# Optimization experiments

Hardware: AMD Instinct MI355X
Metric: run time of the kernel (lower is better)

The kernel has to match this reference:

```python
import jax, jax.numpy as jnp
import numpy as np

RES = 28          # resolution (H == W)
DIM = 384         # channels
NH = 8            # num_heads
HD = DIM // NH    # head_dim = 48
N = RES * RES     # tokens = 784
B = 16            # batch


def _build_bias_idxs(res):
    # Faithful reproduction of the first-occurrence offset indexing in __init__.
    pts = [(i, j) for i in range(res) for j in range(res)]
    offs = {}
    idxs = []
    for p1 in pts:
        for p2 in pts:
            o = (abs(p1[0] - p2[0]), abs(p1[1] - p2[1]))
            if o not in offs:
                offs[o] = len(offs)
            idxs.append(offs[o])
    return np.asarray(idxs, dtype=np.int32).reshape(res * res, res * res), len(offs)


def setup_inputs() -> dict:
    key = jax.random.key(0)
    ks = jax.random.split(key, 6)
    idxs, noff = _build_bias_idxs(RES)  # noff == RES*RES == 784
    s = 0.02
    return {
        "ll": jax.random.normal(ks[0], (B, DIM, RES, RES), jnp.float32),
        "high_attn": jax.random.normal(ks[1], (B, DIM, RES, RES), jnp.float32),
        # 1x1 convs stored as [out_ch, in_ch] matrices
        "q_w": jax.random.normal(ks[2], (DIM, DIM), jnp.float32) * s,
        "q_b": jnp.zeros((DIM,), jnp.float32),
        "kv_w": jax.random.normal(ks[3], (2 * DIM, DIM), jnp.float32) * s,
        "kv_b": jnp.zeros((2 * DIM,), jnp.float32),
        "proj_w": jax.random.normal(ks[4], (DIM, DIM), jnp.float32) * s,
        "proj_b": jnp.zeros((DIM,), jnp.float32),
        "attn_biases": jax.random.normal(ks[5], (NH, noff), jnp.float32) * s,
        "bias_idxs": jnp.asarray(idxs),  # [N, N] int32
    }


def reference(ll, high_attn, q_w, q_b, kv_w, kv_b, proj_w, proj_b, attn_biases, bias_idxs):
    b, c, h, w = ll.shape
    n = h * w
    scale = HD ** -0.5
    # 1x1 convs == per-pixel channel matmuls
    q = jnp.einsum('bchw,oc->bohw', ll, q_w) + q_b[:, None, None]
    kv = jnp.einsum('bchw,oc->bohw', high_attn, kv_w) + kv_b[:, None, None]
    k, v = jnp.split(kv, 2, axis=1)
    q = q.reshape(b, NH, HD, n).transpose(0, 1, 3, 2)  # [B,H,N,hd]
    k = k.reshape(b, NH, HD, n)                        # [B,H,hd,N]
    v = v.reshape(b, NH, HD, n).transpose(0, 1, 3, 2)  # [B,H,N,hd]
    attn = jnp.einsum('bhnd,bhdm->bhnm', q, k) * scale  # [B,H,N,N]
    bias = attn_biases[:, bias_idxs]                    # gather -> [H,N,N]
    attn = jax.nn.softmax(attn + bias[None], axis=-1)
    out = jnp.einsum('bhnm,bhmd->bhnd', attn, v)        # [B,H,N,hd]
    out = out.transpose(0, 1, 3, 2).reshape(b, c, h, w)
    return jnp.einsum('bchw,oc->bohw', out, proj_w) + proj_b[:, None, None]
```

## Files before the change

kernel.cpp:

```cpp
#include <hip/hip_runtime.h>

#define RES    28
#define DIMC   384
#define NHEAD  8
#define HDIM   48
#define DPAD   64
#define NPIX   784
#define NB     16
#define SC2    0.20823294f
#define LOG2E  1.44269504f

typedef short bf16x8 __attribute__((ext_vector_type(8)));
typedef float f32x4  __attribute__((ext_vector_type(4)));

__device__ __forceinline__ short f2bf(float x) {
  union { float f; unsigned u; } v; v.f = x;
  return (short)((v.u + 0x7FFFu + ((v.u >> 16) & 1u)) >> 16);
}
__device__ __forceinline__ unsigned pk_rne(float a, float b) {
  union { float f; unsigned u; } x, y; x.f = a; y.f = b;
  return __builtin_amdgcn_perm(y.u + 0x7FFFu + ((y.u >> 16) & 1u),
                               x.u + 0x7FFFu + ((x.u >> 16) & 1u), 0x07060302u);
}
__device__ __forceinline__ unsigned pk_hu(float a, float b) {
  union { float f; unsigned u; } x, y; x.f = a; y.f = b;
  return __builtin_amdgcn_perm(y.u + 0x8000u, x.u + 0x8000u, 0x07060302u);
}
__device__ __forceinline__ float blo(unsigned u) { union { unsigned u; float f; } v; v.u = u << 16; return v.f; }
__device__ __forceinline__ float bhi(unsigned u) { union { unsigned u; float f; } v; v.u = u & 0xFFFF0000u; return v.f; }


__global__ __launch_bounds__(256) void prep_kernel(
    const float* __restrict__ ll, const float* __restrict__ ha,
    const float* __restrict__ qw, const float* __restrict__ kvw, const float* __restrict__ pw,
    const float* __restrict__ biases,
    short* __restrict__ Xll, short* __restrict__ Xha,
    short* __restrict__ Wf2, short* __restrict__ Wfp,
    short* __restrict__ Bt3, short* __restrict__ Qb,
    short* __restrict__ Kf, short* __restrict__ Vf)
{
  __shared__ __align__(16) short sT[64][72];
  __shared__ float sB[NPIX];
  const int bid = blockIdx.x, t = threadIdx.x;

  if (bid < 2496) {
    const int px = bid % 13, cb = (bid / 13) % 6, zz = bid / 78;
    const int which = zz >> 4, b = zz & 15;
    const float* X = (which ? ha : ll) + (size_t)b * DIMC * NPIX;
    short* T = (which ? Xha : Xll);
    const int c0 = cb * 64, p0 = px * 64;
    const int rrr = t >> 4, pc = (t & 15) * 4;
#pragma unroll
    for (int i = 0; i < 4; ++i) {
      const int c = rrr + 16 * i;
      if (p0 + pc < NPIX) {
        float4 v = *(const float4*)(X + (size_t)(c0 + c) * NPIX + p0 + pc);
        sT[pc + 0][c] = f2bf(v.x); sT[pc + 1][c] = f2bf(v.y);
        sT[pc + 2][c] = f2bf(v.z); sT[pc + 3][c] = f2bf(v.w);
      }
    }
    __syncthreads();
    const int rr = t & 15, qq = (t >> 4) & 3, w = t >> 6;
    const int pxt0 = p0 >> 4, ks0 = c0 >> 5;
#pragma unroll
    for (int i = 0; i < 2; ++i) {
      const int o = w * 2 + i;
      const int pxl = o >> 1, ksl = o & 1;
      if (pxt0 + pxl < 49) {
        short* dst = T + ((size_t)(b * 49 + pxt0 + pxl) * 12 + ks0 + ksl) * 512 + (t & 63) * 8;
        *(bf16x8*)dst = *(const bf16x8*)&sT[pxl * 16 + rr][ksl * 32 + qq * 8];
      }
    }
  } else if (bid < 2784) {
    int gid = (bid - 2496) * 256 + t;
    if (gid < 55296) {
      const int lane = gid & 63;
      const int mt = (gid >> 6) & 7;
      const int ks = (gid >> 9) % 12;
      const int ct = gid / 6144;
      const int chg = ct * 128 + mt * 16 + (lane & 15);
      const int k = ks * 32 + (lane >> 4) * 8;
      const float* src = (chg < DIMC ? qw + (size_t)chg * DIMC
                                     : kvw + (size_t)(chg - DIMC) * DIMC) + k;
      const float4 a = *(const float4*)src;
      const float4 b = *(const float4*)(src + 4);
      bf16x8 o;
      o[0] = f2bf(a.x); o[1] = f2bf(a.y); o[2] = f2bf(a.z); o[3] = f2bf(a.w);
      o[4] = f2bf(b.x); o[5] = f2bf(b.y); o[6] = f2bf(b.z); o[7] = f2bf(b.w);
      *(bf16x8*)(Wf2 + (size_t)gid * 8) = o;
    } else {
      const int g2 = gid - 55296;
      const int lane = g2 & 63;
      const int ks = (g2 >> 6) % 12;
      const int mtile = g2 / 768;
      const int row = mtile * 16 + (lane & 15);
      const int k = ks * 32 + (lane >> 4) * 8;
      const float* src = pw + (size_t)row * DIMC + k;
      const float4 a = *(const float4*)src;
      const float4 b = *(const float4*)(src + 4);
      bf16x8 o;
      o[0] = f2bf(a.x); o[1] = f2bf(a.y); o[2] = f2bf(a.z); o[3] = f2bf(a.w);
      o[4] = f2bf(b.x); o[5] = f2bf(b.y); o[6] = f2bf(b.z); o[7] = f2bf(b.w);
      *(bf16x8*)(Wfp + (size_t)g2 * 8) = o;
    }
  } else if (bid < 3176) {
    const int bb = bid - 2784;
    const int h = bb / 49, qt = bb % 49;
    for (int i = t; i < NPIX; i += 256) sB[i] = biases[h * NPIX + i] * LOG2E;
    __syncthreads();
    const int rr = t & 15, qq = (t >> 4) & 3, w = t >> 6;
    const int qrow = qt * 16 + rr;
    const int i2 = qrow / RES, j2 = qrow - i2 * RES;
    short* dst0 = Bt3 + ((size_t)(h * 49 + qt) * 25) * 512 + (t & 63) * 8;
    const short NEG = f2bf(-1e30f);
    for (int c = w; c < 25; c += 4) {
      short v8[8];
#pragma unroll
      for (int hf = 0; hf < 2; ++hf)
#pragma unroll
        for (int u = 0; u < 4; ++u) {
          const int k = c * 32 + hf * 16 + qq * 4 + u;
          if (k < NPIX) {
            const int i1 = k / RES, j1 = k - i1 * RES;
            int di = i1 - i2; di = di < 0 ? -di : di;
            int dj = j1 - j2; dj = dj < 0 ? -dj : dj;
            v8[hf * 4 + u] = f2bf(sB[di * RES + dj]);
          } else v8[hf * 4 + u] = NEG;
        }
      *(bf16x8*)(dst0 + (size_t)c * 512) = *(const bf16x8*)v8;
    }
  } else {
    const int pp = bid - 3176;
    if (pp < 392) {
      const size_t r = (size_t)pp * 256 + t;
      short* p = Qb + r * DPAD + HDIM;
      *(int4*)p = make_int4(0, 0, 0, 0);
      *(int4*)(p + 8) = make_int4(0, 0, 0, 0);
    } else if (pp < 1192) {
      const int id = (pp - 392) * 256 + t;
      const int l32 = id & 31;
      const int frag = 1 + 2 * ((id >> 5) & 1);
      const int chunk = (id >> 6) % 25;
      const int bh2 = id / 1600;
      short* dst = Kf + (((size_t)bh2 * 25 + chunk) * 4 + frag) * 512 + (32 + l32) * 8;
      *(int4*)dst = make_int4(0, 0, 0, 0);
    } else if (pp < 1256) {
      const int id = (pp - 1192) * 256 + t;
      const int lane2 = id & 63;
      const int frag = 2 + ((id >> 6) & 1);
      const int bh2 = id >> 7;
      short* dst = Kf + (((size_t)bh2 * 25 + 24) * 4 + frag) * 512 + lane2 * 8;
      *(int4*)dst = make_int4(0, 0, 0, 0);
    } else {
      const int id = (pp - 1256) * 256 + t;
      const int bh2 = id / 96;
      const int rem = id - bh2 * 96;
      const int frag = rem >> 5;
      const int l32 = rem & 31;
      short* dst = Vf + (((size_t)bh2 * 25 + 24) * 3 + frag) * 512 + (32 + l32) * 8;
      *(int4*)dst = make_int4(0, 0, 0, 0);
    }
  }
}

__global__ __launch_bounds__(256) void qkv_tiled(
    const short* __restrict__ Wf2, const float* __restrict__ qb, const float* __restrict__ kvb,
    const short* __restrict__ Xll, const short* __restrict__ Xha,
    short* __restrict__ Qb, short* __restrict__ Kf, short* __restrict__ Vf)
{
  __shared__ __align__(16) short sM[15360];
  const int t = threadIdx.x;
  const int w = t >> 6, lane = t & 63;
  const int rr = lane & 15, qq = lane >> 4;
  const int ct = blockIdx.x;
  const int pt = blockIdx.y;
  const int b = pt / 7, pt7 = pt % 7;
  const int px0 = pt7 * 112;

  const short* Xsel = (ct < 3 ? Xll : Xha);
  const short* Bp[7];
#pragma unroll
  for (int pg = 0; pg < 7; ++pg)
    Bp[pg] = Xsel + ((size_t)(b * 49 + pt7 * 7 + pg) * 12) * 512 + lane * 8;

  const short* Ap = Wf2 + (size_t)ct * 12 * 4096 + 2 * w * 512 + lane * 8;

  f32x4 acc[2][7];
#pragma unroll
  for (int mi = 0; mi < 2; ++mi)
#pragma unroll
    for (int pg = 0; pg < 7; ++pg) acc[mi][pg] = (f32x4){0.f, 0.f, 0.f, 0.f};

  bf16x8 a0c = *(const bf16x8*)(Ap);
  bf16x8 a1c = *(const bf16x8*)(Ap + 512);
  bf16x8 bcur[7];
#pragma unroll
  for (int pg = 0; pg < 7; ++pg) bcur[pg] = *(const bf16x8*)(Bp[pg]);

#pragma unroll 2
  for (int s = 0; s < 12; ++s) {
    const int sn = s + (s < 11 ? 1 : 0);
    const short* an = Ap + (size_t)sn * 4096;
    bf16x8 a0n = *(const bf16x8*)(an);
    bf16x8 a1n = *(const bf16x8*)(an + 512);
    bf16x8 bnxt[7];
#pragma unroll
    for (int pg = 0; pg < 7; ++pg) bnxt[pg] = *(const bf16x8*)(Bp[pg] + sn * 512);

#pragma unroll
    for (int pg = 0; pg < 7; ++pg) {
      acc[0][pg] = __builtin_amdgcn_mfma_f32_16x16x32_bf16(a0c, bcur[pg], acc[0][pg], 0, 0, 0);
      acc[1][pg] = __builtin_amdgcn_mfma_f32_16x16x32_bf16(a1c, bcur[pg], acc[1][pg], 0, 0, 0);
    }
    a0c = a0n; a1c = a1n;
#pragma unroll
    for (int pg = 0; pg < 7; ++pg) bcur[pg] = bnxt[pg];
  }

  if (ct < 3) {
#pragma unroll
    for (int mi = 0; mi < 2; ++mi) {
      const int ch = ct * 128 + (2 * w + mi) * 16 + qq * 4;
      const float4 bv = *(const float4*)(qb + ch);
      const int hh = ch / HDIM, d0 = ch % HDIM;
#pragma unroll
      for (int pg = 0; pg < 7; ++pg) {
        const int px = px0 + pg * 16 + rr;
        uint2 pk;
        pk.x = pk_rne(acc[mi][pg][0] + bv.x, acc[mi][pg][1] + bv.y);
        pk.y = pk_rne(acc[mi][pg][2] + bv.z, acc[mi][pg][3] + bv.w);
        *(uint2*)(Qb + (((size_t)b * NHEAD + hh) * NPIX + px) * DPAD + d0) = pk;
      }
    }
  } else if (ct < 6) {
#pragma unroll
    for (int mi = 0; mi < 2; ++mi) {
      const int ch = (ct - 3) * 128 + (2 * w + mi) * 16 + qq * 4;
      const float4 bv = *(const float4*)(kvb + ch);
      const int hh = ch / HDIM, dq = ch % HDIM;
      const int fd = dq >> 5;
      const int laneHi = (dq & 31) >> 3;
      const int elo = dq & 7;
#pragma unroll
      for (int pg = 0; pg < 7; ++pg) {
        const int px = px0 + pg * 16 + rr;
        const int chunk = px >> 5, kh = (px >> 4) & 1;
        uint2 pk;
        pk.x = pk_rne(acc[mi][pg][0] + bv.x, acc[mi][pg][1] + bv.y);
        pk.y = pk_rne(acc[mi][pg][2] + bv.z, acc[mi][pg][3] + bv.w);
        short* dst = Kf + ((((size_t)b * NHEAD + hh) * 25 + chunk) * 4 + kh * 2 + fd) * 512
                     + ((px & 15) + (laneHi << 4)) * 8 + elo;
        *(uint2*)dst = pk;
      }
    }
  } else {
#pragma unroll
    for (int mi = 0; mi < 2; ++mi) {
      const int chl = (2 * w + mi) * 16 + qq * 4;
      const int chv = (ct - 6) * 128 + chl;
      const float4 bv = *(const float4*)(kvb + DIMC + chv);
      const float bb[4] = {bv.x, bv.y, bv.z, bv.w};
#pragma unroll
      for (int pg = 0; pg < 7; ++pg) {
        const int px = pg * 16 + rr;
#pragma unroll
        for (int j = 0; j < 4; ++j)
          sM[(chl + j) * 120 + px] = f2bf(acc[mi][pg][j] + bb[j]);
      }
    }
    __syncthreads();
    for (int id = t; id < 1792; id += 256) {
      const int r = id / 14, o = id - r * 14;
      const int k = px0 + o * 8;
      const int chunk = k >> 5, qv = (k >> 3) & 3;
      const int chv = (ct - 6) * 128 + r;
      const int hh = chv / HDIM, d = chv % HDIM;
      short* dst = Vf + ((((size_t)b * NHEAD + hh) * 25 + chunk) * 3 + (d >> 4)) * 512
                   + ((d & 15) + (qv << 4)) * 8;
      *(bf16x8*)dst = *(const bf16x8*)&sM[r * 120 + o * 8];
    }
  }
}

struct Chain { float sp; f32x4 O0, O1, O2; };

__device__ __forceinline__ void chain_init(Chain& c) {
  c.sp = 0.f;
  c.O0 = (f32x4){0.f,0.f,0.f,0.f}; c.O1 = c.O0; c.O2 = c.O0;
}

__device__ __forceinline__ void chain_step(
    Chain& c, const f32x4 d0, const f32x4 d1, const uint2 bw0, const uint2 bw1,
    short* sPt, const int rr, const int qq)
{
  float s[8];
  s[0] = fmaf(d0[0], SC2, blo(bw0.x)); s[1] = fmaf(d0[1], SC2, bhi(bw0.x));
  s[2] = fmaf(d0[2], SC2, blo(bw0.y)); s[3] = fmaf(d0[3], SC2, bhi(bw0.y));
  s[4] = fmaf(d1[0], SC2, blo(bw1.x)); s[5] = fmaf(d1[1], SC2, bhi(bw1.x));
  s[6] = fmaf(d1[2], SC2, blo(bw1.y)); s[7] = fmaf(d1[3], SC2, bhi(bw1.y));
  float p[8];
#pragma unroll
  for (int j = 0; j < 8; ++j) p[j] = exp2f(fminf(s[j], 30.f));
  const float ss = ((p[0] + p[1]) + (p[2] + p[3])) + ((p[4] + p[5]) + (p[6] + p[7]));
  c.sp += ss;
  uint2 w0; w0.x = pk_hu(p[0], p[1]); w0.y = pk_hu(p[2], p[3]);
  uint2 w1; w1.x = pk_hu(p[4], p[5]); w1.y = pk_hu(p[6], p[7]);
  *(uint2*)(sPt + rr * 40 + qq * 4) = w0;
  *(uint2*)(sPt + rr * 40 + 16 + qq * 4) = w1;
}

__global__ __launch_bounds__(256) void attn_kernel(
    const short* __restrict__ Q, const short* __restrict__ Kf,
    const short* __restrict__ Vf, const short* __restrict__ Bt3,
    short* __restrict__ AOf)
{
  __shared__ __align__(16) char sMem[20480];
  short* sPbase = (short*)sMem;
  const int t = threadIdx.x;
  const int w = t >> 6, lane = t & 63;
  const int rr = lane & 15, qq = lane >> 4;
  const int x = blockIdx.x;
  const int h = x & 7;
  const int i = x >> 3;
  const int b = i / 25, qt = i - b * 25;
  const int qA = qt * 32;
  const bool hasB = (qA + 16 < NPIX);
  const int bh = b * NHEAD + h;

  const short* QpA = Q + ((size_t)bh * NPIX + qA + rr) * DPAD + qq * 8;
  const short* QpB = Q + ((size_t)bh * NPIX + (hasB ? qA + 16 : qA) + rr) * DPAD + qq * 8;
  const bf16x8 qfA0 = *(const bf16x8*)QpA;
  const bf16x8 qfA1 = *(const bf16x8*)(QpA + 32);
  const bf16x8 qfB0 = *(const bf16x8*)QpB;
  const bf16x8 qfB1 = *(const bf16x8*)(QpB + 32);

  const short* Kfp = Kf + (size_t)bh * (25 * 4 * 512) + lane * 8;
  const short* Vfp = Vf + (size_t)bh * (25 * 3 * 512) + lane * 8;
  const short* BpA = Bt3 + ((size_t)(h * 49 + 2 * qt) * 25) * 512 + lane * 8;
  const short* BpB = Bt3 + ((size_t)(h * 49 + (hasB ? 2 * qt + 1 : 2 * qt)) * 25) * 512 + lane * 8;
  short* sPA = sPbase + (w * 2 + 0) * 640;
  short* sPB = sPbase + (w * 2 + 1) * 640;

  Chain cA, cB;
  chain_init(cA); chain_init(cB);

  const int cbeg = w * 6;
  const int cend = (w == 3) ? 25 : cbeg + 6;

  for (int c = cbeg; c < cend; ++c) {
    const short* kc = Kfp + (size_t)c * 2048;
    const bf16x8 ka0 = *(const bf16x8*)kc;
    const bf16x8 ka1 = *(const bf16x8*)(kc + 512);
    const bf16x8 kb0 = *(const bf16x8*)(kc + 1024);
    const bf16x8 kb1 = *(const bf16x8*)(kc + 1536);

    f32x4 dA0 = (f32x4){0.f,0.f,0.f,0.f}, dA1 = dA0, dB0 = dA0, dB1 = dA0;
    dA0 = __builtin_amdgcn_mfma_f32_16x16x32_bf16(ka0, qfA0, dA0, 0, 0, 0);
    dA0 = __builtin_amdgcn_mfma_f32_16x16x32_bf16(ka1, qfA1, dA0, 0, 0, 0);
    dB0 = __builtin_amdgcn_mfma_f32_16x16x32_bf16(ka0, qfB0, dB0, 0, 0, 0);
    dB0 = __builtin_amdgcn_mfma_f32_16x16x32_bf16(ka1, qfB1, dB0, 0, 0, 0);
    dA1 = __builtin_amdgcn_mfma_f32_16x16x32_bf16(kb0, qfA0, dA1, 0, 0, 0);
    dA1 = __builtin_amdgcn_mfma_f32_16x16x32_bf16(kb1, qfA1, dA1, 0, 0, 0);
    dB1 = __builtin_amdgcn_mfma_f32_16x16x32_bf16(kb0, qfB0, dB1, 0, 0, 0);
    dB1 = __builtin_amdgcn_mfma_f32_16x16x32_bf16(kb1, qfB1, dB1, 0, 0, 0);

    const uint4 bA = *(const uint4*)(BpA + (size_t)c * 512);
    const uint4 bB = *(const uint4*)(BpB + (size_t)c * 512);

    chain_step(cA, dA0, dA1, make_uint2(bA.x, bA.y), make_uint2(bA.z, bA.w), sPA, rr, qq);
    chain_step(cB, dB0, dB1, make_uint2(bB.x, bB.y), make_uint2(bB.z, bB.w), sPB, rr, qq);

    const short* vc = Vfp + (size_t)c * 1536;
    const bf16x8 vf0 = *(const bf16x8*)vc;
    const bf16x8 vf1 = *(const bf16x8*)(vc + 512);
    const bf16x8 vf2 = *(const bf16x8*)(vc + 1024);
    const bf16x8 pfA = *(const bf16x8*)(sPA + rr * 40 + qq * 8);
    const bf16x8 pfB = *(const bf16x8*)(sPB + rr * 40 + qq * 8);
    cA.O0 = __builtin_amdgcn_mfma_f32_16x16x32_bf16(vf0, pfA, cA.O0, 0, 0, 0);
    cA.O1 = __builtin_amdgcn_mfma_f32_16x16x32_bf16(vf1, pfA, cA.O1, 0, 0, 0);
    cA.O2 = __builtin_amdgcn_mfma_f32_16x16x32_bf16(vf2, pfA, cA.O2, 0, 0, 0);
    cB.O0 = __builtin_amdgcn_mfma_f32_16x16x32_bf16(vf0, pfB, cB.O0, 0, 0, 0);
    cB.O1 = __builtin_amdgcn_mfma_f32_16x16x32_bf16(vf1, pfB, cB.O1, 0, 0, 0);
    cB.O2 = __builtin_amdgcn_mfma_f32_16x16x32_bf16(vf2, pfB, cB.O2, 0, 0, 0);
  }

  __syncthreads();
  float* mbuf = (float*)sMem;
  if (w > 0) {
    const int col = ((w - 1) * 2 + 0) * 64 + lane;
    const int colB = col + 64;
    float vals[13] = {cA.O0[0], cA.O0[1], cA.O0[2], cA.O0[3],
                      cA.O1[0], cA.O1[1], cA.O1[2], cA.O1[3],
                      cA.O2[0], cA.O2[1], cA.O2[2], cA.O2[3], cA.sp};
    float valsB[13] = {cB.O0[0], cB.O0[1], cB.O0[2], cB.O0[3],
                       cB.O1[0], cB.O1[1], cB.O1[2], cB.O1[3],
                       cB.O2[0], cB.O2[1], cB.O2[2], cB.O2[3], cB.sp};
#pragma unroll
    for (int j = 0; j < 13; ++j) mbuf[j * 384 + col] = vals[j];
#pragma unroll
    for (int j = 0; j < 13; ++j) mbuf[j * 384 + colB] = valsB[j];
  }
  __syncthreads();
  if (w != 0) return;

#pragma unroll
  for (int ww = 0; ww < 3; ++ww) {
    const int col = (ww * 2 + 0) * 64 + lane;
    const int colB = col + 64;
#pragma unroll
    for (int j = 0; j < 4; ++j) {
      cA.O0[j] += mbuf[j * 384 + col];
      cA.O1[j] += mbuf[(4 + j) * 384 + col];
      cA.O2[j] += mbuf[(8 + j) * 384 + col];
      cB.O0[j] += mbuf[j * 384 + colB];
      cB.O1[j] += mbuf[(4 + j) * 384 + colB];
      cB.O2[j] += mbuf[(8 + j) * 384 + colB];
    }
    cA.sp += mbuf[12 * 384 + col];
    cB.sp += mbuf[12 * 384 + colB];
  }

  {
    float sA = cA.sp;
    sA += __shfl_xor(sA, 16); sA += __shfl_xor(sA, 32);
    const float invA = 1.f / sA;
    const f32x4 OA[3] = {cA.O0, cA.O1, cA.O2};
    short* base = AOf + ((size_t)(b * 49 + 2 * qt) * 12) * 512;
#pragma unroll
    for (int part = 0; part < 3; ++part) {
      const int ch = h * HDIM + part * 16 + qq * 4;
      uint2 pk;
      pk.x = pk_rne(OA[part][0] * invA, OA[part][1] * invA);
      pk.y = pk_rne(OA[part][2] * invA, OA[part][3] * invA);
      short* dst = base + (ch >> 5) * 512 + (rr + (((ch >> 3) & 3) << 4)) * 8 + (ch & 7);
      *(uint2*)dst = pk;
    }
  }
  if (hasB) {
    float sB2 = cB.sp;
    sB2 += __shfl_xor(sB2, 16); sB2 += __shfl_xor(sB2, 32);
    const float invB = 1.f / sB2;
    const f32x4 OB[3] = {cB.O0, cB.O1, cB.O2};
    short* base = AOf + ((size_t)(b * 49 + 2 * qt + 1) * 12) * 512;
#pragma unroll
    for (int part = 0; part < 3; ++part) {
      const int ch = h * HDIM + part * 16 + qq * 4;
      uint2 pk;
      pk.x = pk_rne(OB[part][0] * invB, OB[part][1] * invB);
      pk.y = pk_rne(OB[part][2] * invB, OB[part][3] * invB);
      short* dst = base + (ch >> 5) * 512 + (rr + (((ch >> 3) & 3) << 4)) * 8 + (ch & 7);
      *(uint2*)dst = pk;
    }
  }
}

__global__ __launch_bounds__(256) void proj_gemm(
    const short* __restrict__ Wfp, const float* __restrict__ pb,
    const short* __restrict__ AOf, float* __restrict__ out)
{
  const int t = threadIdx.x;
  const int w = t >> 6, lane = t & 63;
  const int rr = lane & 15, qq = lane >> 4;
  const int b = blockIdx.y;
  const int bx = blockIdx.x;
  const int pix = bx * 16 + rr;

  const short* Xp = AOf + ((size_t)(b * 49 + bx) * 12) * 512 + lane * 8;
  const short* wfp = Wfp + ((size_t)w * 12 * 64 + lane) * 8;

  f32x4 acc[6];
#pragma unroll
  for (int i = 0; i < 6; ++i) acc[i] = (f32x4){0.f, 0.f, 0.f, 0.f};

  bf16x8 xfc = *(const bf16x8*)(Xp);
  bf16x8 afc[6];
#pragma unroll
  for (int i = 0; i < 6; ++i) afc[i] = *(const bf16x8*)(wfp + (size_t)i * 24576);

#pragma unroll 2
  for (int ks = 0; ks < 12; ++ks) {
    const int kn = ks + (ks < 11 ? 1 : 0);
    const bf16x8 xfn = *(const bf16x8*)(Xp + kn * 512);
    bf16x8 afn[6];
#pragma unroll
    for (int i = 0; i < 6; ++i)
      afn[i] = *(const bf16x8*)(wfp + (size_t)i * 24576 + kn * 512);

#pragma unroll
    for (int i = 0; i < 6; ++i)
      acc[i] = __builtin_amdgcn_mfma_f32_16x16x32_bf16(afc[i], xfc, acc[i], 0, 0, 0);

    xfc = xfn;
#pragma unroll
    for (int i = 0; i < 6; ++i) afc[i] = afn[i];
  }
#pragma unroll
  for (int i = 0; i < 6; ++i) {
    const int ch0 = (w + 4 * i) * 16 + qq * 4;
    const float4 bv = *(const float4*)(pb + ch0);
    float* o = out + ((size_t)b * DIMC + ch0) * NPIX + pix;
    o[0] = acc[i][0] + bv.x;
    o[NPIX] = acc[i][1] + bv.y;
    o[2 * NPIX] = acc[i][2] + bv.z;
    o[3 * NPIX] = acc[i][3] + bv.w;
  }
}

extern "C" void kernel_launch(void* const* d_in, const int* in_sizes, int n_in,
                              void* d_out, int out_size, void* d_ws, size_t ws_size,
                              hipStream_t stream)
{
  const float* ll     = (const float*)d_in[0];
  const float* ha     = (const float*)d_in[1];
  const float* q_w    = (const float*)d_in[2];
  const float* q_b    = (const float*)d_in[3];
  const float* kv_w   = (const float*)d_in[4];
  const float* kv_b   = (const float*)d_in[5];
  const float* proj_w = (const float*)d_in[6];
  const float* proj_b = (const float*)d_in[7];
  const float* biases = (const float*)d_in[8];
  float* out = (float*)d_out;

  short* Qb  = (short*)d_ws;
  short* Kf  = Qb  + (size_t)NB * NHEAD * NPIX * DPAD;
  short* Vf  = Kf  + (size_t)128 * 25 * 4 * 512;
  short* Xll = Vf  + (size_t)128 * 25 * 3 * 512;
  short* Xha = Xll + (size_t)NB * 49 * 12 * 512;
  short* AOf = Xha + (size_t)NB * 49 * 12 * 512;
  short* Bt3 = AOf + (size_t)NB * 49 * 12 * 512;
  short* Wf2 = Bt3 + (size_t)NHEAD * 49 * 25 * 512;
  short* Wfp = Wf2 + (size_t)55296 * 8;

  prep_kernel<<<dim3(4480), 256, 0, stream>>>(ll, ha, q_w, kv_w, proj_w, biases,
                                              Xll, Xha, Wf2, Wfp, Bt3, Qb, Kf, Vf);
  qkv_tiled<<<dim3(9, 112), 256, 0, stream>>>(Wf2, q_b, kv_b, Xll, Xha, Qb, Kf, Vf);
  attn_kernel<<<dim3(3200), 256, 0, stream>>>(Qb, Kf, Vf, Bt3, AOf);
  proj_gemm<<<dim3(49, NB), 256, 0, stream>>>(Wfp, proj_b, AOf, out);
}
```

Measured before the change: 197.4 us.

## Stage QKV activations through LDS via async loads, add MFMA priority, drop exp clamp

The QKV projection kernel now double-buffers the activation tiles in shared memory using global_load_lds, so the 7 pixel groups are loaded once per block and shared across the four waves. Before, each wave loaded all of them into registers itself. This adds a __syncthreads per k-step. The attention kernel wraps its MFMA bursts in s_setprio so matrix work gets issue priority over other waves. It also removes the fminf clamp before exp2f, which drops one instruction per element but gives up protection against overflow for large scores.

```diff
diff --git a/kernel.cpp b/kernel.cpp
--- a/kernel.cpp
+++ b/kernel.cpp
@@ -178,10 +178,7 @@
   const int px0 = pt7 * 112;
 
   const short* Xsel = (ct < 3 ? Xll : Xha);
-  const short* Bp[7];
-#pragma unroll
-  for (int pg = 0; pg < 7; ++pg)
-    Bp[pg] = Xsel + ((size_t)(b * 49 + pt7 * 7 + pg) * 12) * 512 + lane * 8;
+  const int xt0 = b * 49 + pt7 * 7;
 
   const short* Ap = Wf2 + (size_t)ct * 12 * 4096 + 2 * w * 512 + lane * 8;
 
@@ -191,30 +188,41 @@
 #pragma unroll
     for (int pg = 0; pg < 7; ++pg) acc[mi][pg] = (f32x4){0.f, 0.f, 0.f, 0.f};
 
+  auto stageB = [&](int buf, int s) {
+    short* l0 = &sM[buf * 3584 + w * 512];
+    const short* g0 = Xsel + ((size_t)(xt0 + w) * 12 + s) * 512 + lane * 8;
+    __builtin_amdgcn_global_load_lds((const __attribute__((address_space(1))) void*)g0,
+                                     (__attribute__((address_space(3))) void*)l0, 16, 0, 0);
+    if (w < 3) {
+      short* l1 = &sM[buf * 3584 + (w + 4) * 512];
+      const short* g1 = Xsel + ((size_t)(xt0 + w + 4) * 12 + s) * 512 + lane * 8;
+      __builtin_amdgcn_global_load_lds((const __attribute__((address_space(1))) void*)g1,
+                                       (__attribute__((address_space(3))) void*)l1, 16, 0, 0);
+    }
+  };
+
+  stageB(0, 0);
   bf16x8 a0c = *(const bf16x8*)(Ap);
   bf16x8 a1c = *(const bf16x8*)(Ap + 512);
-  bf16x8 bcur[7];
-#pragma unroll
-  for (int pg = 0; pg < 7; ++pg) bcur[pg] = *(const bf16x8*)(Bp[pg]);
-
-#pragma unroll 2
+  __syncthreads();
+
   for (int s = 0; s < 12; ++s) {
-    const int sn = s + (s < 11 ? 1 : 0);
+    const int buf = s & 1;
+    if (s < 11) stageB(buf ^ 1, s + 1);
+    const int sn = s < 11 ? s + 1 : s;
     const short* an = Ap + (size_t)sn * 4096;
-    bf16x8 a0n = *(const bf16x8*)(an);
-    bf16x8 a1n = *(const bf16x8*)(an + 512);
-    bf16x8 bnxt[7];
-#pragma unroll
-    for (int pg = 0; pg < 7; ++pg) bnxt[pg] = *(const bf16x8*)(Bp[pg] + sn * 512);
-
+    const bf16x8 a0n = *(const bf16x8*)(an);
+    const bf16x8 a1n = *(const bf16x8*)(an + 512);
+
+    const short* sBb = &sM[buf * 3584];
 #pragma unroll
     for (int pg = 0; pg < 7; ++pg) {
-      acc[0][pg] = __builtin_amdgcn_mfma_f32_16x16x32_bf16(a0c, bcur[pg], acc[0][pg], 0, 0, 0);
-      acc[1][pg] = __builtin_amdgcn_mfma_f32_16x16x32_bf16(a1c, bcur[pg], acc[1][pg], 0, 0, 0);
+      const bf16x8 bf = *(const bf16x8*)(sBb + pg * 512 + lane * 8);
+      acc[0][pg] = __builtin_amdgcn_mfma_f32_16x16x32_bf16(a0c, bf, acc[0][pg], 0, 0, 0);
+      acc[1][pg] = __builtin_amdgcn_mfma_f32_16x16x32_bf16(a1c, bf, acc[1][pg], 0, 0, 0);
     }
     a0c = a0n; a1c = a1n;
-#pragma unroll
-    for (int pg = 0; pg < 7; ++pg) bcur[pg] = bnxt[pg];
+    __syncthreads();
   }
 
   if (ct < 3) {
@@ -300,7 +308,7 @@
   s[6] = fmaf(d1[2], SC2, blo(bw1.y)); s[7] = fmaf(d1[3], SC2, bhi(bw1.y));
   float p[8];
 #pragma unroll
-  for (int j = 0; j < 8; ++j) p[j] = exp2f(fminf(s[j], 30.f));
+  for (int j = 0; j < 8; ++j) p[j] = exp2f(s[j]);
   const float ss = ((p[0] + p[1]) + (p[2] + p[3])) + ((p[4] + p[5]) + (p[6] + p[7]));
   c.sp += ss;
   uint2 w0; w0.x = pk_hu(p[0], p[1]); w0.y = pk_hu(p[2], p[3]);
@@ -355,6 +363,7 @@
     const bf16x8 kb1 = *(const bf16x8*)(kc + 1536);
 
     f32x4 dA0 = (f32x4){0.f,0.f,0.f,0.f}, dA1 = dA0, dB0 = dA0, dB1 = dA0;
+    __builtin_amdgcn_s_setprio(1);
     dA0 = __builtin_amdgcn_mfma_f32_16x16x32_bf16(ka0, qfA0, dA0, 0, 0, 0);
     dA0 = __builtin_amdgcn_mfma_f32_16x16x32_bf16(ka1, qfA1, dA0, 0, 0, 0);
     dB0 = __builtin_amdgcn_mfma_f32_16x16x32_bf16(ka0, qfB0, dB0, 0, 0, 0);
@@ -363,6 +372,7 @@
     dA1 = __builtin_amdgcn_mfma_f32_16x16x32_bf16(kb1, qfA1, dA1, 0, 0, 0);
     dB1 = __builtin_amdgcn_mfma_f32_16x16x32_bf16(kb0, qfB0, dB1, 0, 0, 0);
     dB1 = __builtin_amdgcn_mfma_f32_16x16x32_bf16(kb1, qfB1, dB1, 0, 0, 0);
+    __builtin_amdgcn_s_setprio(0);
 
     const uint4 bA = *(const uint4*)(BpA + (size_t)c * 512);
     const uint4 bB = *(const uint4*)(BpB + (size_t)c * 512);
@@ -376,12 +386,14 @@
     const bf16x8 vf2 = *(const bf16x8*)(vc + 1024);
     const bf16x8 pfA = *(const bf16x8*)(sPA + rr * 40 + qq * 8);
     const bf16x8 pfB = *(const bf16x8*)(sPB + rr * 40 + qq * 8);
+    __builtin_amdgcn_s_setprio(1);
     cA.O0 = __builtin_amdgcn_mfma_f32_16x16x32_bf16(vf0, pfA, cA.O0, 0, 0, 0);
     cA.O1 = __builtin_amdgcn_mfma_f32_16x16x32_bf16(vf1, pfA, cA.O1, 0, 0, 0);
     cA.O2 = __builtin_amdgcn_mfma_f32_16x16x32_bf16(vf2, pfA, cA.O2, 0, 0, 0);
     cB.O0 = __builtin_amdgcn_mfma_f32_16x16x32_bf16(vf0, pfB, cB.O0, 0, 0, 0);
     cB.O1 = __builtin_amdgcn_mfma_f32_16x16x32_bf16(vf1, pfB, cB.O1, 0, 0, 0);
     cB.O2 = __builtin_amdgcn_mfma_f32_16x16x32_bf16(vf2, pfB, cB.O2, 0, 0, 0);
+    __builtin_amdgcn_s_setprio(0);
   }
 
   __syncthreads();
```

Measured after the change: 193.8 us. No clear change (-1.9%).
